# Kernel optimization log

Hardware: AMD Instinct MI355X
Metric: run time of the kernel (lower is better)

## Reference

```python
import jax, jax.numpy as jnp
import numpy as np

N = 1048576  # n_envs (patients)

# param column order in the (N,30) params array
_P = ['BW','KMAX','B','D','KMIN','KABS','F','KP1','KP2','KP3','FSNC','KE1','KE2',
     'K1','K2','VM0','VMX','KM0','M1','M2','M4','KA1','KA2','VI','P2U','IB','KI',
     'M30','KD','KSC']
_IDX = {n: i for i, n in enumerate(_P)}


def setup_inputs() -> dict:
    key = jax.random.key(0)
    ks = jax.random.split(key, 6)
    # positive, well-conditioned values (B < 1, divisors bounded away from 0)
    x = jax.random.uniform(ks[0], (N, 13), jnp.float32, 0.1, 2.0)
    params = jax.random.uniform(ks[1], (N, 30), jnp.float32, 0.5, 0.95)
    action_ins = jax.random.uniform(ks[2], (N, 1), jnp.float32, 0.0, 1.0)
    action_CHO = jax.random.uniform(ks[3], (N, 1), jnp.float32, 0.0, 1.0)
    last_Qsto = jax.random.uniform(ks[4], (N, 1), jnp.float32, 0.0, 1.0)
    last_foodtaken = jax.random.uniform(ks[5], (N, 1), jnp.float32, 0.0, 1.0)
    return {'x': x, 'params': params, 'action_ins': action_ins,
            'action_CHO': action_CHO, 'last_Qsto': last_Qsto,
            'last_foodtaken': last_foodtaken}


def _dxdt(x, params, action_ins, action_CHO, last_Qsto, last_foodtaken):
    p = lambda n: params[:, _IDX[n]:_IDX[n] + 1]  # (N,1) column
    xs = [x[:, i:i + 1] for i in range(13)]

    BW = p('BW'); KMAX = p('KMAX'); B = p('B'); D = p('D'); KMIN = p('KMIN')
    KABS = p('KABS'); F = p('F'); KP1 = p('KP1'); KP2 = p('KP2'); KP3 = p('KP3')
    FSNC = p('FSNC'); KE1 = p('KE1'); KE2 = p('KE2'); K1 = p('K1'); K2 = p('K2')
    VM0 = p('VM0'); VMX = p('VMX'); KM0 = p('KM0'); M1 = p('M1'); M2 = p('M2')
    M4 = p('M4'); KA1 = p('KA1'); KA2 = p('KA2'); VI = p('VI'); P2U = p('P2U')
    IB = p('IB'); KI = p('KI'); M30 = p('M30'); KD = p('KD'); KSC = p('KSC')

    f_insulin = action_ins * 6000.0 / BW
    qsto = xs[0] + xs[1]
    Dbar = last_Qsto + last_foodtaken

    dx0 = -KMAX * xs[0] + action_CHO * 1000.0

    aa = 5.0 / 2.0 / (1.0 - B) / (Dbar + 1e-7)
    cc = 5.0 / 2.0 / D / (Dbar + 1e-7)
    kgut_true = KMIN + (KMAX - KMIN) / 2.0 * (
        jnp.tanh(aa * (qsto - B * Dbar)) - jnp.tanh(cc * (qsto - D * Dbar)) + 2.0)
    kgut = jnp.where(Dbar > 0, kgut_true, KMAX)

    dx1 = KMAX * xs[0] - xs[1] * kgut
    dx2 = kgut * xs[1] - KABS * xs[2]

    Rat = F * KABS * xs[2] / BW
    EGPt = KP1 - KP2 * xs[3] - KP3 * xs[8]
    Et = jnp.where(xs[3] > KE2, KE1 * (xs[3] - KE2), 0.0)
    dx3 = jnp.maximum(EGPt, 0.0) + Rat - FSNC - Et - K1 * xs[3] + K2 * xs[4]
    dx3 = jnp.where(xs[3] >= 0, dx3, 0.0)

    Vmt = VM0 + VMX * xs[6]
    Uidt = Vmt * xs[4] / (KM0 + xs[4])
    dx4 = -Uidt + K1 * xs[3] - K2 * xs[4]
    dx4 = jnp.where(xs[4] >= 0, dx4, 0.0)

    dx5 = -(M2 + M4) * xs[5] + M1 * xs[9] + KA1 * xs[10] + KA2 * xs[11]
    It = xs[5] / VI
    dx5 = jnp.where(xs[5] >= 0, dx5, 0.0)

    dx6 = -P2U * xs[6] + P2U * (It - IB)
    dx7 = -KI * (xs[7] - It)
    dx8 = -KI * (xs[8] - xs[7])

    dx9 = -(M1 + M30) * xs[9] + M2 * xs[5]
    dx9 = jnp.where(xs[9] >= 0, dx9, 0.0)

    dx10 = f_insulin - (KA1 + KD) * xs[10]
    dx10 = jnp.where(xs[10] >= 0, dx10, 0.0)

    dx11 = KD * xs[10] - KA2 * xs[11]
    dx11 = jnp.where(xs[11] >= 0, dx11, 0.0)

    dx12 = -KSC * xs[12] + KSC * xs[3]
    dx12 = jnp.where(xs[12] >= 0, dx12, 0.0)

    return jnp.concatenate(
        [dx0, dx1, dx2, dx3, dx4, dx5, dx6, dx7, dx8, dx9, dx10, dx11, dx12],
        axis=1)  # (N, 13)


def reference(x, params, action_ins, action_CHO, last_Qsto, last_foodtaken):
    return _dxdt(x, params, action_ins, action_CHO, last_Qsto, last_foodtaken)
```

## Files before the change

kernel.cpp:

```cpp
#include <hip/hip_runtime.h>
#include <math.h>

#define BLOCK 256
#define XW 13
#define PW 30

__device__ __forceinline__ void dxdt(const float* X, const float* P,
                                     float ai, float cho, float lq, float lf,
                                     float* dx)
{
    const float BW = P[0],  KMAX = P[1],  B   = P[2],  D   = P[3],  KMIN = P[4];
    const float KABS = P[5], F   = P[6],  KP1 = P[7],  KP2 = P[8],  KP3  = P[9];
    const float FSNC = P[10], KE1 = P[11], KE2 = P[12], K1 = P[13], K2   = P[14];
    const float VM0 = P[15], VMX = P[16], KM0 = P[17], M1 = P[18], M2   = P[19];
    const float M4  = P[20], KA1 = P[21], KA2 = P[22], VI = P[23], P2U  = P[24];
    const float IB  = P[25], KI  = P[26], M30 = P[27], KD = P[28], KSC  = P[29];

    const float f_insulin = ai * 6000.0f / BW;
    const float qsto = X[0] + X[1];
    const float Dbar = lq + lf;

    dx[0] = -KMAX * X[0] + cho * 1000.0f;

    const float inv_dbar = 1.0f / (Dbar + 1e-7f);
    const float aa = 2.5f / (1.0f - B) * inv_dbar;
    const float cc = 2.5f / D * inv_dbar;
    const float kgut_true = KMIN + (KMAX - KMIN) * 0.5f *
        (tanhf(aa * (qsto - B * Dbar)) - tanhf(cc * (qsto - D * Dbar)) + 2.0f);
    const float kgut = (Dbar > 0.0f) ? kgut_true : KMAX;

    dx[1] = KMAX * X[0] - X[1] * kgut;
    dx[2] = kgut * X[1] - KABS * X[2];

    const float Rat  = F * KABS * X[2] / BW;
    const float EGPt = KP1 - KP2 * X[3] - KP3 * X[8];
    const float Et   = (X[3] > KE2) ? KE1 * (X[3] - KE2) : 0.0f;
    const float d3 = fmaxf(EGPt, 0.0f) + Rat - FSNC - Et - K1 * X[3] + K2 * X[4];
    dx[3] = (X[3] >= 0.0f) ? d3 : 0.0f;

    const float Vmt  = VM0 + VMX * X[6];
    const float Uidt = Vmt * X[4] / (KM0 + X[4]);
    const float d4 = -Uidt + K1 * X[3] - K2 * X[4];
    dx[4] = (X[4] >= 0.0f) ? d4 : 0.0f;

    const float d5 = -(M2 + M4) * X[5] + M1 * X[9] + KA1 * X[10] + KA2 * X[11];
    const float It = X[5] / VI;
    dx[5] = (X[5] >= 0.0f) ? d5 : 0.0f;

    dx[6] = -P2U * X[6] + P2U * (It - IB);
    dx[7] = -KI * (X[7] - It);
    dx[8] = -KI * (X[8] - X[7]);

    const float d9 = -(M1 + M30) * X[9] + M2 * X[5];
    dx[9] = (X[9] >= 0.0f) ? d9 : 0.0f;

    const float d10 = f_insulin - (KA1 + KD) * X[10];
    dx[10] = (X[10] >= 0.0f) ? d10 : 0.0f;

    const float d11 = KD * X[10] - KA2 * X[11];
    dx[11] = (X[11] >= 0.0f) ? d11 : 0.0f;

    const float d12 = -KSC * X[12] + KSC * X[3];
    dx[12] = (X[12] >= 0.0f) ? d12 : 0.0f;
}

__global__ __launch_bounds__(BLOCK) void t1d_kernel(
    const float* __restrict__ x,
    const float* __restrict__ params,
    const float* __restrict__ action_ins,
    const float* __restrict__ action_CHO,
    const float* __restrict__ last_Qsto,
    const float* __restrict__ last_foodtaken,
    float* __restrict__ out, int n)
{
    __shared__ float xbuf[BLOCK * XW];
    __shared__ float pbuf[BLOCK * PW];

    const int tid = threadIdx.x;
    const size_t base = (size_t)blockIdx.x * BLOCK;

    if (base + BLOCK <= (size_t)n) {
        const float4* xg = (const float4*)(x + base * XW);
        float4*       xl = (float4*)xbuf;
        for (int k = tid; k < BLOCK * XW / 4; k += BLOCK)
            xl[k] = xg[k];
        const float4* pg = (const float4*)(params + base * PW);
        float4*       pl = (float4*)pbuf;
        for (int k = tid; k < BLOCK * PW / 4; k += BLOCK)
            pl[k] = pg[k];

        const float ai  = action_ins[base + tid];
        const float cho = action_CHO[base + tid];
        const float lq  = last_Qsto[base + tid];
        const float lf  = last_foodtaken[base + tid];

        __syncthreads();

        float X[XW], P[PW], dx[XW];
        #pragma unroll
        for (int j = 0; j < XW; ++j) X[j] = xbuf[tid * XW + j];
        #pragma unroll
        for (int j = 0; j < PW; ++j) P[j] = pbuf[tid * PW + j];

        dxdt(X, P, ai, cho, lq, lf, dx);

        #pragma unroll
        for (int j = 0; j < XW; ++j) xbuf[tid * XW + j] = dx[j];

        __syncthreads();

        float4* og = (float4*)(out + base * XW);
        for (int k = tid; k < BLOCK * XW / 4; k += BLOCK)
            og[k] = xl[k];
    } else {
        const size_t i = base + tid;
        if (i < (size_t)n) {
            float X[XW], P[PW], dx[XW];
            #pragma unroll
            for (int j = 0; j < XW; ++j) X[j] = x[i * XW + j];
            #pragma unroll
            for (int j = 0; j < PW; ++j) P[j] = params[i * PW + j];
            dxdt(X, P, action_ins[i], action_CHO[i], last_Qsto[i],
                 last_foodtaken[i], dx);
            #pragma unroll
            for (int j = 0; j < XW; ++j) out[i * XW + j] = dx[j];
        }
    }
}

extern "C" void kernel_launch(void* const* d_in, const int* in_sizes, int n_in,
                              void* d_out, int out_size, void* d_ws, size_t ws_size,
                              hipStream_t stream) {
    const float* x      = (const float*)d_in[0];
    const float* params = (const float*)d_in[1];
    const float* ai     = (const float*)d_in[2];
    const float* cho    = (const float*)d_in[3];
    const float* lq     = (const float*)d_in[4];
    const float* lf     = (const float*)d_in[5];
    float* out = (float*)d_out;

    const int n = in_sizes[0] / XW;
    const int grid = (n + BLOCK - 1) / BLOCK;
    t1d_kernel<<<grid, BLOCK, 0, stream>>>(x, params, ai, cho, lq, lf, out, n);
}
```

Measured before the change: 254.0 us.

## Use single-wave blocks to drop barriers and batch staging loads

Switches from 256-thread blocks to single 64-lane wavefront blocks, which removes the __syncthreads barriers around the shared-memory staging. All global float4 loads are issued up front into registers before being written to LDS, which gives more memory-level parallelism per wave. The risk is that the code relies on implicit wave-level ordering of LDS accesses without any barrier or fence, and that the grid becomes four times larger with smaller blocks.

```diff
diff --git a/kernel.cpp b/kernel.cpp
--- a/kernel.cpp
+++ b/kernel.cpp
@@ -1,7 +1,7 @@
 #include <hip/hip_runtime.h>
 #include <math.h>
 
-#define BLOCK 256
+#define WAVE 64
 #define XW 13
 #define PW 30
 
@@ -64,7 +64,7 @@
     dx[12] = (X[12] >= 0.0f) ? d12 : 0.0f;
 }
 
-__global__ __launch_bounds__(BLOCK) void t1d_kernel(
+__global__ __launch_bounds__(WAVE, 4) void t1d_kernel(
     const float* __restrict__ x,
     const float* __restrict__ params,
     const float* __restrict__ action_ins,
@@ -73,47 +73,72 @@
     const float* __restrict__ last_foodtaken,
     float* __restrict__ out, int n)
 {
-    __shared__ float xbuf[BLOCK * XW];
-    __shared__ float pbuf[BLOCK * PW];
+    __shared__ float xb[WAVE * XW];
+    __shared__ float pb[WAVE * PW];
 
-    const int tid = threadIdx.x;
-    const size_t base = (size_t)blockIdx.x * BLOCK;
+    const int l = threadIdx.x;
+    const size_t base = (size_t)blockIdx.x * WAVE;
 
-    if (base + BLOCK <= (size_t)n) {
+    if (base + WAVE <= (size_t)n) {
         const float4* xg = (const float4*)(x + base * XW);
-        float4*       xl = (float4*)xbuf;
-        for (int k = tid; k < BLOCK * XW / 4; k += BLOCK)
-            xl[k] = xg[k];
         const float4* pg = (const float4*)(params + base * PW);
-        float4*       pl = (float4*)pbuf;
-        for (int k = tid; k < BLOCK * PW / 4; k += BLOCK)
-            pl[k] = pg[k];
+        float4* xl4 = (float4*)xb;
+        float4* pl4 = (float4*)pb;
 
-        const float ai  = action_ins[base + tid];
-        const float cho = action_CHO[base + tid];
-        const float lq  = last_Qsto[base + tid];
-        const float lf  = last_foodtaken[base + tid];
+        float4 a0 = xg[l];
+        float4 a1 = xg[l + 64];
+        float4 a2 = xg[l + 128];
+        float4 a3; if (l < 16) a3 = xg[192 + l];
 
-        __syncthreads();
+        float4 b0 = pg[l];
+        float4 b1 = pg[l + 64];
+        float4 b2 = pg[l + 128];
+        float4 b3 = pg[l + 192];
+        float4 b4 = pg[l + 256];
+        float4 b5 = pg[l + 320];
+        float4 b6 = pg[l + 384];
+        float4 b7; if (l < 32) b7 = pg[448 + l];
+
+        const float ai  = action_ins[base + l];
+        const float cho = action_CHO[base + l];
+        const float lq  = last_Qsto[base + l];
+        const float lf  = last_foodtaken[base + l];
+
+        xl4[l]       = a0;
+        xl4[l + 64]  = a1;
+        xl4[l + 128] = a2;
+        if (l < 16) xl4[192 + l] = a3;
+        pl4[l]       = b0;
+        pl4[l + 64]  = b1;
+        pl4[l + 128] = b2;
+        pl4[l + 192] = b3;
+        pl4[l + 256] = b4;
+        pl4[l + 320] = b5;
+        pl4[l + 384] = b6;
+        if (l < 32) pl4[448 + l] = b7;
 
         float X[XW], P[PW], dx[XW];
         #pragma unroll
-        for (int j = 0; j < XW; ++j) X[j] = xbuf[tid * XW + j];
+        for (int j = 0; j < XW; ++j) X[j] = xb[l * XW + j];
         #pragma unroll
-        for (int j = 0; j < PW; ++j) P[j] = pbuf[tid * PW + j];
+        for (int j = 0; j < PW; ++j) P[j] = pb[l * PW + j];
 
         dxdt(X, P, ai, cho, lq, lf, dx);
 
         #pragma unroll
-        for (int j = 0; j < XW; ++j) xbuf[tid * XW + j] = dx[j];
+        for (int j = 0; j < XW; ++j) xb[l * XW + j] = dx[j];
 
-        __syncthreads();
-
+        float4 o0 = xl4[l];
+        float4 o1 = xl4[l + 64];
+        float4 o2 = xl4[l + 128];
+        float4 o3; if (l < 16) o3 = xl4[192 + l];
         float4* og = (float4*)(out + base * XW);
-        for (int k = tid; k < BLOCK * XW / 4; k += BLOCK)
-            og[k] = xl[k];
+        og[l]       = o0;
+        og[l + 64]  = o1;
+        og[l + 128] = o2;
+        if (l < 16) og[192 + l] = o3;
     } else {
-        const size_t i = base + tid;
+        const size_t i = base + l;
         if (i < (size_t)n) {
             float X[XW], P[PW], dx[XW];
             #pragma unroll
@@ -140,6 +165,6 @@
     float* out = (float*)d_out;
 
     const int n = in_sizes[0] / XW;
-    const int grid = (n + BLOCK - 1) / BLOCK;
-    t1d_kernel<<<grid, BLOCK, 0, stream>>>(x, params, ai, cho, lq, lf, out, n);
+    const int grid = (n + WAVE - 1) / WAVE;
+    t1d_kernel<<<grid, WAVE, 0, stream>>>(x, params, ai, cho, lq, lf, out, n);
 }
```

After: 247.6 us. 2.5% less time.
